# Performance work log

Measured on AMD Instinct MI355X. Metric: run time of the kernel, lower is better.

The kernel has to match this reference:

```python
import jax, jax.numpy as jnp
import numpy as np

CTX, SP, HIST, NC = 168, 24, 336, 128
LAGS = [24, 48, 72, 96, 120, 144, 168, 0]  # lags_seq + [0]
NSEG = CTX // SP  # 7


def gru_cell(x, h, Wih, Whh, bih, bhh):
    # torch.nn.GRUCell math; x: (N, D), h: (N, H)
    gi = x @ Wih.T + bih
    gh = h @ Whh.T + bhh
    ir, iz, inn = jnp.split(gi, 3, axis=-1)
    hr, hz, hn = jnp.split(gh, 3, axis=-1)
    r = jax.nn.sigmoid(ir + hr)
    z = jax.nn.sigmoid(iz + hz)
    n = jnp.tanh(inn + r * hn)
    return (1.0 - z) * n + z * h


def lstm(x, h, c, Wih, Whh, b):
    # single-layer batch_first LSTM; x: (B, T, D); torch gate order i,f,g,o
    xw = jnp.einsum('btd,gd->btg', x, Wih) + b  # precompute input projection
    def step(carry, xt):
        h, c = carry
        gates = xt + h @ Whh.T
        i, f, g, o = jnp.split(gates, 4, axis=-1)
        c = jax.nn.sigmoid(f) * c + jax.nn.sigmoid(i) * jnp.tanh(g)
        h = jax.nn.sigmoid(o) * jnp.tanh(c)
        return (h, c), h
    (h, c), ys = jax.lax.scan(step, (h, c), jnp.swapaxes(xw, 0, 1))
    return jnp.swapaxes(ys, 0, 1), h, c


def setup_inputs() -> dict:
    key = jax.random.key(0)
    ks = jax.random.split(key, 20)
    B = 8192
    p = lambda k, shape: jax.random.normal(k, shape, jnp.float32) * 0.05
    return dict(
        feat_static_cat=jax.random.randint(ks[0], (B, 1), 0, 50),
        feat_static_real=jax.random.normal(ks[1], (B, 1), jnp.float32),
        past_time_feat=jax.random.normal(ks[2], (B, HIST, 4), jnp.float32),
        past_target=jax.random.uniform(ks[3], (B, HIST), jnp.float32),
        past_observed_values=jnp.ones((B, HIST), jnp.float32),
        future_time_feat=jax.random.normal(ks[4], (B, SP, 4), jnp.float32),
        emb_table=p(ks[5], (50, 16)),
        gru_Wih=p(ks[6], (3 * NC, 30)),
        gru_Whh=p(ks[7], (3 * NC, NC)),
        gru_bih=p(ks[8], (3 * NC,)),
        gru_bhh=p(ks[9], (3 * NC,)),
        enc_Wih=p(ks[10], (NSEG, 4 * NC, NC)),
        enc_Whh=p(ks[11], (NSEG, 4 * NC, NC)),
        enc_b=p(ks[12], (NSEG, 4 * NC)),
        dec_Wih=p(ks[13], (4 * NC, 180)),
        dec_Whh=p(ks[14], (4 * NC, NC)),
        dec_b=p(ks[15], (4 * NC,)),
        out_W=p(ks[16], (1, NC)),
        out_b=p(ks[17], (1,)),
    )


def reference(feat_static_cat, feat_static_real, past_time_feat, past_target,
              past_observed_values, future_time_feat,
              emb_table, gru_Wih, gru_Whh, gru_bih, gru_bhh,
              enc_Wih, enc_Whh, enc_b, dec_Wih, dec_Whh, dec_b,
              out_W, out_b):
    B = past_target.shape[0]
    time_feat = past_time_feat[:, HIST - CTX:, :]  # (B, CTX, 4)

    # lagged subsequences: lagged[:, j, k] = seq[:, HIST - lag_k - CTX + j]
    lags = jnp.stack(
        [past_target[:, HIST - lag - CTX: HIST - lag] for lag in LAGS], axis=-1
    )  # (B, CTX, 8)

    # MeanScaler over past_target[:, CTX:] (keepdim)
    data = past_target[:, CTX:]
    w = past_observed_values[:, CTX:]
    total_w = w.sum(axis=1)                     # (B,)
    wsum = (jnp.abs(data) * w).sum(axis=1)      # (B,)
    default_scale = wsum.sum() / jnp.maximum(total_w.sum(), 1.0)
    scale = wsum / jnp.maximum(total_w, 1.0)
    scale = jnp.maximum(1e-10, jnp.where(wsum > 0, scale, default_scale))
    scale = scale[:, None]                      # (B, 1)

    embedded = emb_table[feat_static_cat[:, 0]]  # (B, 16)
    static_feat = jnp.concatenate([embedded, feat_static_real, jnp.log(scale)], axis=1)  # (B, 18)
    rep_static = jnp.broadcast_to(static_feat[:, None, :], (B, CTX, static_feat.shape[-1]))

    lags_scaled = lags / scale[:, :, None]
    inputs = jnp.concatenate([lags_scaled, time_feat, rep_static], axis=-1)  # (B, CTX, 30)
    inputs = inputs.reshape(B, NSEG, SP, inputs.shape[-1])  # (B, 7, 24, 30)

    encoder_out = jnp.zeros((B, SP, NC), inputs.dtype)
    h = jnp.zeros((B, NC), inputs.dtype)
    c = jnp.zeros((B, NC), inputs.dtype)
    for i in range(NSEG):  # fixed small loop; each segment has distinct LSTM weights
        x = inputs[:, i].reshape(-1, inputs.shape[-1])  # (B*SP, 30)
        hv = gru_cell(x, encoder_out.reshape(-1, NC), gru_Wih, gru_Whh, gru_bih, gru_bhh)
        hv = hv.reshape(B, SP, NC)
        encoder_out, h, c = lstm(hv, h, c, enc_Wih[i], enc_Whh[i], enc_b[i])

    query = jnp.concatenate(
        [inputs[:, 0], encoder_out, future_time_feat, rep_static[:, -SP:, :]], axis=-1
    )  # (B, 24, 180)
    dec_out, _, _ = lstm(query, h, c, dec_Wih, dec_Whh, dec_b)
    outputs = dec_out @ out_W.T + out_b  # (B, 24, 1)
    return outputs * scale[:, :, None]
```

## Files before the change

### kernel.cpp

```cpp
#include <hip/hip_runtime.h>
#include <math.h>

typedef short bf16x8 __attribute__((ext_vector_type(8)));
typedef float f32x4 __attribute__((ext_vector_type(4)));
typedef unsigned short u16;
typedef unsigned int u32;

#define WSUMS 0
#define TOTWS 1
#define WSUM_OFF 2
#define TOTW_OFF 8194
#define SCL_F 16386
#define WB_BYTE 98432

#define GWI_U 0
#define GWH_U 12288
#define EO_U  61440
#define DO_U  978944
#define XG_U  1142784
#define XD_U  23162880

#define L2E 1.4426950408889634f
#define T2E 2.8853900817779268f

__constant__ int cLAG[8] = {144,120,96,72,48,24,0,168};

__device__ __forceinline__ float sig2(float x){
  return __builtin_amdgcn_rcpf(1.0f+__builtin_amdgcn_exp2f(-x));
}
__device__ __forceinline__ float th2(float x){
  return __builtin_fmaf(-2.0f, __builtin_amdgcn_rcpf(__builtin_amdgcn_exp2f(x)+1.0f), 1.0f);
}
__device__ __forceinline__ float thc(float x){
  return th2(x*T2E);
}
__device__ __forceinline__ u16 f2b(float x){ u32 u=__float_as_uint(x); return (u16)((u + 0x7fffu + ((u>>16)&1u))>>16); }
__device__ __forceinline__ float b2f(u16 v){ return __uint_as_float(((u32)v)<<16); }
__device__ __forceinline__ u32 f2b_pk(float lo, float hi){
  u32 r; asm("v_cvt_pk_bf16_f32 %0, %1, %2" : "=v"(r) : "v"(lo), "v"(hi)); return r;
}
__device__ __forceinline__ void pin(bf16x8 &x){
  f32x4 t = __builtin_bit_cast(f32x4, x);
  asm volatile("" : "+v"(t));
  x = __builtin_bit_cast(bf16x8, t);
}

#define MFMA(a,b,c) __builtin_amdgcn_mfma_f32_16x16x32_bf16(a,b,c,0,0,0)

__global__ void scale_kernel(const float* __restrict__ tgt,
                             const float* __restrict__ obs,
                             float* __restrict__ ws)
{
  __shared__ float s1[256], s2[256];
  int b = blockIdx.x*256 + threadIdx.x;
  float wsum=0.f, totw=0.f;
  const float* tr = tgt + b*336 + 168;
  const float* wr = obs + b*336 + 168;
  for(int t=0;t<168;t++){ float w=wr[t]; wsum += fabsf(tr[t])*w; totw += w; }
  ws[WSUM_OFF + b] = wsum;
  ws[TOTW_OFF + b] = totw;
  s1[threadIdx.x]=wsum; s2[threadIdx.x]=totw;
  __syncthreads();
  for(int s=128;s>0;s>>=1){
    if(threadIdx.x<s){ s1[threadIdx.x]+=s1[threadIdx.x+s]; s2[threadIdx.x]+=s2[threadIdx.x+s]; }
    __syncthreads();
  }
  if(threadIdx.x==0){ atomicAdd(&ws[WSUMS], s1[0]); atomicAdd(&ws[TOTWS], s2[0]); }
}

__global__ void prep_w(const float* __restrict__ gWih, const float* __restrict__ gWhh,
                       const float* __restrict__ eWih, const float* __restrict__ eWhh,
                       const float* __restrict__ dWih, const float* __restrict__ dWhh,
                       float* __restrict__ ws)
{
  u16* WU = (u16*)((char*)ws + WB_BYTE);
  int tid = blockIdx.x*blockDim.x + threadIdx.x;
  int nt = gridDim.x*blockDim.x;
  for(int i=tid;i<12288;i+=nt){ int n=i>>5,k=i&31;
    float s=((n>>7)==2)?T2E:L2E;
    WU[GWI_U+i]=(k<30)?f2b(gWih[n*30+k]*s):(u16)0; }
  for(int i=tid;i<49152;i+=nt){ int n=i>>7,k=i&127;
    float s=((n>>7)==2)?T2E:L2E;
    WU[GWH_U+i]=f2b(gWhh[n*128+k]*s); }
  for(int i=tid;i<917504;i+=nt){
    int s=i>>17,r2=i&131071,n=r2>>8,k=r2&255;
    float sc=((n>>7)==2)?T2E:L2E;
    float v=(k<128)?eWih[(s*512+n)*128+k]:eWhh[(s*512+n)*128+(k-128)];
    WU[EO_U+i]=f2b(v*sc);
  }
  for(int i=tid;i<163840;i+=nt){
    int n=i/320, k=i-n*320; float v;
    float sc=((n>>7)==2)?T2E:L2E;
    if(k<128)       v=dWih[n*180+30+k];
    else if(k<136)  v=dWih[n*180+(k-128)];
    else if(k<140)  v=dWih[n*180+8+(k-136)];
    else if(k<144)  v=dWih[n*180+158+(k-140)];
    else if(k<162)  v=dWih[n*180+12+(k-144)];
    else if(k<180)  v=dWih[n*180+162+(k-162)];
    else if(k<192)  v=0.f;
    else            v=dWhh[n*128+(k-192)];
    WU[DO_U+i]=f2b(v*sc);
  }
}

__global__ void prep_x(const float* __restrict__ tgt, const float* __restrict__ ptf,
                       const float* __restrict__ ftf, float* __restrict__ ws)
{
  __shared__ float inv_l[64];
  u16* WU = (u16*)((char*)ws + WB_BYTE);
  const int tid = threadIdx.x;
  const int b0 = blockIdx.x*64;
  if(tid<64){
    int b=b0+tid;
    float wsumv=ws[WSUM_OFF+b], totw=ws[TOTW_OFF+b];
    float def=ws[WSUMS]/fmaxf(ws[TOTWS],1.f);
    float sc=fmaxf(1e-10f,(wsumv>0.f)?wsumv/fmaxf(totw,1.f):def);
    ws[SCL_F+b]=sc; inv_l[tid]=1.f/sc;
  }
  __syncthreads();
  for(int idx=tid; idx<64*168; idx+=256){
    int bl=idx/168, gt=idx-bl*168; int b=b0+bl;
    float iv=inv_l[bl];
    __align__(16) u16 row[16];
    #pragma unroll
    for(int j=0;j<8;j++) row[j]=f2b(tgt[b*336+cLAG[j]+gt]*iv);
    const float* pp=ptf+((size_t)(b*336+168+gt))*4;
    #pragma unroll
    for(int j=0;j<4;j++) row[8+j]=f2b(pp[j]);
    row[12]=row[13]=row[14]=row[15]=0;
    int seg=gt/24, t=gt-seg*24;
    u16* dst=WU+XG_U+(((size_t)seg*8192+b)*24+t)*16;
    *(uint4*)dst=*(const uint4*)row; *(uint4*)(dst+8)=*(const uint4*)(row+8);
  }
  for(int idx=tid; idx<64*24; idx+=256){
    int bl=idx/24, t=idx-bl*24; int b=b0+bl;
    float iv=inv_l[bl];
    __align__(16) u16 row[16];
    #pragma unroll
    for(int j=0;j<8;j++) row[j]=f2b(tgt[b*336+cLAG[j]+t]*iv);
    #pragma unroll
    for(int j=0;j<4;j++) row[8+j]=f2b(ptf[((size_t)(b*336+168+t))*4+j]);
    #pragma unroll
    for(int j=0;j<4;j++) row[12+j]=f2b(ftf[b*96+t*4+j]);
    u16* dst=WU+XD_U+((size_t)b*24+t)*16;
    *(uint4*)dst=*(const uint4*)row; *(uint4*)(dst+8)=*(const uint4*)(row+8);
  }
}

__global__ __launch_bounds__(512,2)
__attribute__((amdgpu_waves_per_eu(2,2)))
void deepar_main(const int* __restrict__ cat, const float* __restrict__ sreal,
                 const float* __restrict__ emb,
                 const float* __restrict__ gbih, const float* __restrict__ gbhh,
                 const float* __restrict__ encb, const float* __restrict__ decb,
                 const float* __restrict__ outW, const float* __restrict__ outb,
                 float* __restrict__ ws, float* __restrict__ out)
{
  asm volatile("" ::: "v252","v253","v254","v255");

  const u16* __restrict__ WU=(const u16*)((const char*)ws+WB_BYTE);

  __shared__ __align__(16) u16 encbuf[384*136];
  __shared__ __align__(16) u16 Xast[4][64*40];
  __shared__ __align__(16) u16 Xdast[2][16*72];
  __shared__ __align__(16) u16 hstash[2][16*136];
  __shared__ u16 statb[16][18];
  __shared__ float scl_s[16];
  __shared__ float outw_s[128];
  __shared__ float red[16][8];
  __shared__ float outb_s;

  const int tid=threadIdx.x;
  const int b0=blockIdx.x*16;
  const int wv=tid>>6, lane=tid&63, quad=lane>>4, l15=lane&15;
  const int ccol=wv*16+quad*4;

  auto stageX = [&](int gc){
    if(tid<128 && gc<42){
      int sg=gc/6, cc=gc-sg*6;
      int a=tid>>1;
      u16* Xb=&Xast[gc&3][0];
      const u16* src=WU+XG_U+(((size_t)sg*8192+b0+(a>>2))*24+4*cc+(a&3))*16;
      if(tid&1) *(uint2*)(Xb+a*40+8)=*(const uint2*)(src+8);
      else      *(uint4*)(Xb+a*40)  =*(const uint4*)src;
    }
  };

  if(tid<16) scl_s[tid]=ws[SCL_F+b0+tid];
  if(tid<128) outw_s[tid]=outW[tid];
  if(tid==128) outb_s=outb[0];
  if(tid>=256){ int q=tid-256; int r=q>>4,k=q&15; statb[r][k]=f2b(emb[cat[b0+r]*16+k]); }
  { const uint4 z4={0,0,0,0};
    for(int i=tid;i<6528;i+=512) *(uint4*)(encbuf+i*8)=z4;
    for(int i=tid;i<544;i+=512)  *(uint4*)(&hstash[0][0]+i*8)=z4;
  }
  __syncthreads();
  if(tid<16){ statb[tid][16]=f2b(sreal[b0+tid]); statb[tid][17]=f2b(logf(scl_s[tid])); }
  __syncthreads();
  for(int i=tid;i<1280;i+=512){ int a=i/20, k=i-a*20+12;
    u16 v=(k<30)?statb[a>>2][k-12]:(u16)0;
    Xast[0][a*40+k]=v; Xast[1][a*40+k]=v; Xast[2][a*40+k]=v; Xast[3][a*40+k]=v; }
  for(int i=tid;i<896;i+=512){ int rr=i/56, k=i-rr*56+16;
    u16 v; if(k<34) v=statb[rr][k-16]; else if(k<52) v=statb[rr][k-34]; else v=0;
    Xdast[0][rr*72+k]=v; Xdast[1][rr*72+k]=v; }
  stageX(0); stageX(1);
  __syncthreads();

  f32x4 b4r, b4z, b4i2, b4h2;
  {
    float4 bi0=*(const float4*)(gbih+(wv    )*16+quad*4);
    float4 bh0=*(const float4*)(gbhh+(wv    )*16+quad*4);
    float4 bi1=*(const float4*)(gbih+(wv+ 8)*16+quad*4);
    float4 bh1=*(const float4*)(gbhh+(wv+ 8)*16+quad*4);
    float4 bi2=*(const float4*)(gbih+(wv+16)*16+quad*4);
    float4 bh2=*(const float4*)(gbhh+(wv+16)*16+quad*4);
    b4r =(f32x4){(bi0.x+bh0.x)*L2E,(bi0.y+bh0.y)*L2E,(bi0.z+bh0.z)*L2E,(bi0.w+bh0.w)*L2E};
    b4z =(f32x4){(bi1.x+bh1.x)*L2E,(bi1.y+bh1.y)*L2E,(bi1.z+bh1.z)*L2E,(bi1.w+bh1.w)*L2E};
    b4i2=(f32x4){bi2.x*T2E,bi2.y*T2E,bi2.z*T2E,bi2.w*T2E};
    b4h2=(f32x4){bh2.x*T2E,bh2.y*T2E,bh2.z*T2E,bh2.w*T2E};
  }

  float cst[4]={0.f,0.f,0.f,0.f};
  int p=0;

  for(int seg=0;seg<7;seg++){
    bf16x8 gwi[3]; bf16x8 gwh[3][4];
    #pragma unroll
    for(int j=0;j<3;j++){
      int nb=(wv+j*8)*16+l15;
      gwi[j]=*(const bf16x8*)(WU+GWI_U+nb*32+quad*8); pin(gwi[j]);
      #pragma unroll
      for(int kt=0;kt<4;kt++){ gwh[j][kt]=*(const bf16x8*)(WU+GWH_U+nb*128+kt*32+quad*8); pin(gwh[j][kt]); }
    }

    for(int c=0;c<6;c++){
      stageX(seg*6+c+2);
      const u16* Xb = &Xast[(seg*6+c)&3][0];

      f32x4 g01[2][4], a2[4], h2[4];
      #pragma unroll
      for(int mt=0;mt<4;mt++){
        bf16x8 af=*(const bf16x8*)(Xb+(mt*16+l15)*40+quad*8);
        g01[0][mt]=MFMA(gwi[0],af,b4r);
        g01[1][mt]=MFMA(gwi[1],af,b4z);
        a2[mt]   =MFMA(gwi[2],af,b4i2);
      }
      const u16* ebase=encbuf+(size_t)(c*64)*136;
      #pragma unroll
      for(int kt=0;kt<4;kt++)
        #pragma unroll
        for(int mt=0;mt<4;mt++){
          bf16x8 af=*(const bf16x8*)(ebase+(mt*16+l15)*136+kt*32+quad*8);
          g01[0][mt]=MFMA(gwh[0][kt],af,g01[0][mt]);
          g01[1][mt]=MFMA(gwh[1][kt],af,g01[1][mt]);
          h2[mt]   =MFMA(gwh[2][kt],af,(kt==0)?b4h2:h2[mt]);
        }
      uint2 hv2[4];
      #pragma unroll
      for(int mt=0;mt<4;mt++){
        uint2 hp2=*(const uint2*)(ebase+(size_t)(mt*16+l15)*136+ccol);
        float hv[4];
        #pragma unroll
        for(int reg=0;reg<4;reg++){
          float rg=sig2(g01[0][mt][reg]);
          float zg=sig2(g01[1][mt][reg]);
          u32 w=(reg&2)?hp2.y:hp2.x;
          float hp=b2f((u16)((reg&1)?(w>>16):w));
          float nn=th2(__builtin_fmaf(rg,h2[mt][reg],a2[mt][reg]));
          hv[reg]=__builtin_fmaf(zg,hp-nn,nn);
        }
        hv2[mt].x=f2b_pk(hv[0],hv[1]);
        hv2[mt].y=f2b_pk(hv[2],hv[3]);
      }
      __syncthreads();
      #pragma unroll
      for(int mt=0;mt<4;mt++)
        *(uint2*)(encbuf+(size_t)(c*64+mt*16+l15)*136+ccol)=hv2[mt];
    }

    bf16x8 we[4][8]; f32x4 b4e[4];
    #pragma unroll
    for(int j=0;j<4;j++){
      float s=(j==2)?T2E:L2E;
      float4 bb=*(const float4*)(encb+seg*512+(wv+j*8)*16+quad*4);
      b4e[j]=(f32x4){bb.x*s,bb.y*s,bb.z*s,bb.w*s};
      int nb=(wv+j*8)*16+l15;
      #pragma unroll
      for(int kt=0;kt<8;kt++){
        we[j][kt]=*(const bf16x8*)(WU+EO_U+(size_t)seg*131072+nb*256+kt*32+quad*8);
        pin(we[j][kt]);
      }
    }
    uint2 hprev2={0,0}; int tbprev=0;
    for(int t=0;t<24;t++){
      int tb=(t>>2)*64+(t&3);
      __syncthreads();
      const u16* Hb=&hstash[p][0];
      const u16* Ar=encbuf+(size_t)(tb+l15*4)*136;
      f32x4 acc[4];
      #pragma unroll
      for(int kt=0;kt<8;kt++){
        bf16x8 af=(kt<4)? *(const bf16x8*)(Ar+kt*32+quad*8)
                        : *(const bf16x8*)(Hb+l15*136+(kt-4)*32+quad*8);
        #pragma unroll
        for(int j=0;j<4;j++) acc[j]=MFMA(we[j][kt],af,(kt==0)?b4e[j]:acc[j]);
      }
      if(t>0)
        *(uint2*)(encbuf+(size_t)(tbprev+l15*4)*136+ccol)=hprev2;
      { float hf[4];
        #pragma unroll
        for(int reg=0;reg<4;reg++){
          float ig=sig2(acc[0][reg]),fg=sig2(acc[1][reg]);
          float gg=th2(acc[2][reg]), og=sig2(acc[3][reg]);
          float c_=__builtin_fmaf(fg,cst[reg],ig*gg); cst[reg]=c_;
          hf[reg]=og*thc(c_);
        }
        hprev2.x=f2b_pk(hf[0],hf[1]);
        hprev2.y=f2b_pk(hf[2],hf[3]);
      }
      int pn=p^1;
      *(uint2*)(&hstash[pn][0]+(size_t)l15*136+ccol)=hprev2;
      tbprev=tb; p=pn;
    }
    *(uint2*)(encbuf+(size_t)(tbprev+l15*4)*136+ccol)=hprev2;
  }

  bf16x8 wd[4][10]; f32x4 b4d[4];
  #pragma unroll
  for(int j=0;j<4;j++){
    float s=(j==2)?T2E:L2E;
    float4 bb=*(const float4*)(decb+(wv+j*8)*16+quad*4);
    b4d[j]=(f32x4){bb.x*s,bb.y*s,bb.z*s,bb.w*s};
    int nb=(wv+j*8)*16+l15;
    #pragma unroll
    for(int kt=0;kt<10;kt++){
      wd[j][kt]=*(const bf16x8*)(WU+DO_U+nb*320+kt*32+quad*8);
      pin(wd[j][kt]);
    }
  }
  if(tid>=256 && tid<288){ int q=tid-256; int rr=q>>1;
    const u16* src=WU+XD_U+((size_t)(b0+rr)*24+0)*16;
    u16* Xw=&Xdast[0][0];
    if(q&1) *(uint4*)(Xw+rr*72+8)=*(const uint4*)(src+8);
    else    *(uint4*)(Xw+rr*72)  =*(const uint4*)src; }
  __syncthreads();
  for(int t=0;t<24;t++){
    int tb=(t>>2)*64+(t&3);
    const u16* Ar=encbuf+(size_t)(tb+l15*4)*136;
    const u16* Xd=&Xdast[t&1][0];
    const u16* Hb=&hstash[p][0];
    f32x4 acc[4];
    #pragma unroll
    for(int kt=0;kt<10;kt++){
      bf16x8 af=(kt<4)? *(const bf16x8*)(Ar+kt*32+quad*8)
              :(kt<6)? *(const bf16x8*)(Xd+l15*72+(kt-4)*32+quad*8)
                     : *(const bf16x8*)(Hb+l15*136+(kt-6)*32+quad*8);
      #pragma unroll
      for(int j=0;j<4;j++) acc[j]=MFMA(wd[j][kt],af,(kt==0)?b4d[j]:acc[j]);
    }
    if(t<23 && tid>=256 && tid<288){ int q=tid-256; int rr=q>>1;
      const u16* src=WU+XD_U+((size_t)(b0+rr)*24+t+1)*16;
      u16* Xw=&Xdast[(t+1)&1][0];
      if(q&1) *(uint4*)(Xw+rr*72+8)=*(const uint4*)(src+8);
      else    *(uint4*)(Xw+rr*72)  =*(const uint4*)src; }
    uint2 hnew2;
    { float hf[4];
      #pragma unroll
      for(int reg=0;reg<4;reg++){
        float ig=sig2(acc[0][reg]),fg=sig2(acc[1][reg]);
        float gg=th2(acc[2][reg]), og=sig2(acc[3][reg]);
        float c_=__builtin_fmaf(fg,cst[reg],ig*gg); cst[reg]=c_;
        hf[reg]=og*thc(c_);
      }
      hnew2.x=f2b_pk(hf[0],hf[1]);
      hnew2.y=f2b_pk(hf[2],hf[3]);
    }
    int pn=p^1;
    *(uint2*)(&hstash[pn][0]+(size_t)l15*136+ccol)=hnew2;
    __syncthreads();
    if(tid<128){ int row=tid>>3,g=tid&7; float s=0.f;
      #pragma unroll
      for(int i=0;i<16;i++) s+=b2f(hstash[pn][row*136+g*16+i])*outw_s[g*16+i];
      red[row][g]=s; }
    __syncthreads();
    if(tid<16){ float s=outb_s;
      #pragma unroll
      for(int g=0;g<8;g++) s+=red[tid][g];
      out[(b0+tid)*24+t]=s*scl_s[tid]; }
    p=pn;
  }
}

extern "C" void kernel_launch(void* const* d_in, const int* in_sizes, int n_in,
                              void* d_out, int out_size, void* d_ws, size_t ws_size,
                              hipStream_t stream)
{
  (void)in_sizes; (void)n_in; (void)out_size; (void)ws_size;
  const int*   cat  = (const int*)d_in[0];
  const float* sreal= (const float*)d_in[1];
  const float* ptf  = (const float*)d_in[2];
  const float* tgt  = (const float*)d_in[3];
  const float* obs  = (const float*)d_in[4];
  const float* ftf  = (const float*)d_in[5];
  const float* emb  = (const float*)d_in[6];
  const float* gWih = (const float*)d_in[7];
  const float* gWhh = (const float*)d_in[8];
  const float* gbih = (const float*)d_in[9];
  const float* gbhh = (const float*)d_in[10];
  const float* eWih = (const float*)d_in[11];
  const float* eWhh = (const float*)d_in[12];
  const float* encb = (const float*)d_in[13];
  const float* dWih = (const float*)d_in[14];
  const float* dWhh = (const float*)d_in[15];
  const float* decb = (const float*)d_in[16];
  const float* outW = (const float*)d_in[17];
  const float* outb = (const float*)d_in[18];
  float* ws  = (float*)d_ws;
  float* out = (float*)d_out;

  hipMemsetAsync(d_ws, 0, 2*sizeof(float), stream);
  scale_kernel<<<dim3(8192/256), dim3(256), 0, stream>>>(tgt, obs, ws);
  prep_w<<<dim3(512), dim3(256), 0, stream>>>(gWih,gWhh,eWih,eWhh,dWih,dWhh,ws);
  prep_x<<<dim3(128), dim3(256), 0, stream>>>(tgt, ptf, ftf, ws);
  deepar_main<<<dim3(512), dim3(512), 0, stream>>>(cat,sreal,emb,gbih,gbhh,encb,decb,
                                                   outW,outb,ws,out);
}
```

Before: 897.3 us.

## Split LSTM gate accumulators, pad LDS rows, fuse output projection into gate epilogue

Widens the LDS row stride for encbuf and hstash from 136 to 140 elements, meant to cut bank conflicts on the fragment loads. In the encoder and decoder LSTM steps, the single serial MFMA accumulation chain is split into two independent chains (input part and hidden part) that are summed before the gates, giving more instruction-level parallelism. The decoder output projection now uses per-thread fp32 partial dot products written to a double-buffered reduction array, which removes one __syncthreads and the separate reduction pass per step. It costs a few extra adds, more LDS, and a slightly different fp32 (not bf16-rounded) output sum.

Result: slower. 1.499 ms (+67.1%).

```diff
diff --git a/kernel.cpp b/kernel.cpp
--- a/kernel.cpp
+++ b/kernel.cpp
@@ -22,6 +22,8 @@
 
 #define L2E 1.4426950408889634f
 #define T2E 2.8853900817779268f
+
+#define EROW 140
 
 __constant__ int cLAG[8] = {144,120,96,72,48,24,0,168};
 
@@ -160,20 +162,20 @@
 
   const u16* __restrict__ WU=(const u16*)((const char*)ws+WB_BYTE);
 
-  __shared__ __align__(16) u16 encbuf[384*136];
+  __shared__ __align__(16) u16 encbuf[384*EROW];
   __shared__ __align__(16) u16 Xast[4][64*40];
   __shared__ __align__(16) u16 Xdast[2][16*72];
-  __shared__ __align__(16) u16 hstash[2][16*136];
+  __shared__ __align__(16) u16 hstash[2][16*EROW];
   __shared__ u16 statb[16][18];
   __shared__ float scl_s[16];
-  __shared__ float outw_s[128];
-  __shared__ float red[16][8];
+  __shared__ float red2[2][16][32];
   __shared__ float outb_s;
 
   const int tid=threadIdx.x;
   const int b0=blockIdx.x*16;
   const int wv=tid>>6, lane=tid&63, quad=lane>>4, l15=lane&15;
   const int ccol=wv*16+quad*4;
+  const f32x4 zz={0.f,0.f,0.f,0.f};
 
   auto stageX = [&](int gc){
     if(tid<128 && gc<42){
@@ -187,13 +189,13 @@
   };
 
   if(tid<16) scl_s[tid]=ws[SCL_F+b0+tid];
-  if(tid<128) outw_s[tid]=outW[tid];
   if(tid==128) outb_s=outb[0];
   if(tid>=256){ int q=tid-256; int r=q>>4,k=q&15; statb[r][k]=f2b(emb[cat[b0+r]*16+k]); }
   { const uint4 z4={0,0,0,0};
-    for(int i=tid;i<6528;i+=512) *(uint4*)(encbuf+i*8)=z4;
-    for(int i=tid;i<544;i+=512)  *(uint4*)(&hstash[0][0]+i*8)=z4;
-  }
+    for(int i=tid;i<6720;i+=512) *(uint4*)(encbuf+i*8)=z4;
+    for(int i=tid;i<560;i+=512)  *(uint4*)(&hstash[0][0]+i*8)=z4;
+  }
+  const float4 ow=*(const float4*)(outW+ccol);
   __syncthreads();
   if(tid<16){ statb[tid][16]=f2b(sreal[b0+tid]); statb[tid][17]=f2b(logf(scl_s[tid])); }
   __syncthreads();
@@ -245,12 +247,12 @@
         g01[1][mt]=MFMA(gwi[1],af,b4z);
         a2[mt]   =MFMA(gwi[2],af,b4i2);
       }
-      const u16* ebase=encbuf+(size_t)(c*64)*136;
+      const u16* ebase=encbuf+(size_t)(c*64)*EROW;
       #pragma unroll
       for(int kt=0;kt<4;kt++)
         #pragma unroll
         for(int mt=0;mt<4;mt++){
-          bf16x8 af=*(const bf16x8*)(ebase+(mt*16+l15)*136+kt*32+quad*8);
+          bf16x8 af=*(const bf16x8*)(ebase+(mt*16+l15)*EROW+kt*32+quad*8);
           g01[0][mt]=MFMA(gwh[0][kt],af,g01[0][mt]);
           g01[1][mt]=MFMA(gwh[1][kt],af,g01[1][mt]);
           h2[mt]   =MFMA(gwh[2][kt],af,(kt==0)?b4h2:h2[mt]);
@@ -258,7 +260,7 @@
       uint2 hv2[4];
       #pragma unroll
       for(int mt=0;mt<4;mt++){
-        uint2 hp2=*(const uint2*)(ebase+(size_t)(mt*16+l15)*136+ccol);
+        uint2 hp2=*(const uint2*)(ebase+(size_t)(mt*16+l15)*EROW+ccol);
         float hv[4];
         #pragma unroll
         for(int reg=0;reg<4;reg++){
@@ -275,7 +277,7 @@
       __syncthreads();
       #pragma unroll
       for(int mt=0;mt<4;mt++)
-        *(uint2*)(encbuf+(size_t)(c*64+mt*16+l15)*136+ccol)=hv2[mt];
+        *(uint2*)(encbuf+(size_t)(c*64+mt*16+l15)*EROW+ccol)=hv2[mt];
     }
 
     bf16x8 we[4][8]; f32x4 b4e[4];
@@ -296,22 +298,27 @@
       int tb=(t>>2)*64+(t&3);
       __syncthreads();
       const u16* Hb=&hstash[p][0];
-      const u16* Ar=encbuf+(size_t)(tb+l15*4)*136;
-      f32x4 acc[4];
-      #pragma unroll
-      for(int kt=0;kt<8;kt++){
-        bf16x8 af=(kt<4)? *(const bf16x8*)(Ar+kt*32+quad*8)
-                        : *(const bf16x8*)(Hb+l15*136+(kt-4)*32+quad*8);
+      const u16* Ar=encbuf+(size_t)(tb+l15*4)*EROW;
+      f32x4 aA[4], aH[4];
+      #pragma unroll
+      for(int kt=0;kt<4;kt++){
+        bf16x8 afA=*(const bf16x8*)(Ar+kt*32+quad*8);
+        bf16x8 afH=*(const bf16x8*)(Hb+l15*EROW+kt*32+quad*8);
         #pragma unroll
-        for(int j=0;j<4;j++) acc[j]=MFMA(we[j][kt],af,(kt==0)?b4e[j]:acc[j]);
+        for(int j=0;j<4;j++){
+          aA[j]=MFMA(we[j][kt],afA,(kt==0)?b4e[j]:aA[j]);
+          aH[j]=MFMA(we[j][kt+4],afH,(kt==0)?zz:aH[j]);
+        }
       }
       if(t>0)
-        *(uint2*)(encbuf+(size_t)(tbprev+l15*4)*136+ccol)=hprev2;
+        *(uint2*)(encbuf+(size_t)(tbprev+l15*4)*EROW+ccol)=hprev2;
       { float hf[4];
         #pragma unroll
         for(int reg=0;reg<4;reg++){
-          float ig=sig2(acc[0][reg]),fg=sig2(acc[1][reg]);
-          float gg=th2(acc[2][reg]), og=sig2(acc[3][reg]);
+          float a0=aA[0][reg]+aH[0][reg], a1=aA[1][reg]+aH[1][reg];
+          float a2v=aA[2][reg]+aH[2][reg], a3=aA[3][reg]+aH[3][reg];
+          float ig=sig2(a0),fg=sig2(a1);
+          float gg=th2(a2v), og=sig2(a3);
           float c_=__builtin_fmaf(fg,cst[reg],ig*gg); cst[reg]=c_;
           hf[reg]=og*thc(c_);
         }
@@ -319,10 +326,10 @@
         hprev2.y=f2b_pk(hf[2],hf[3]);
       }
       int pn=p^1;
-      *(uint2*)(&hstash[pn][0]+(size_t)l15*136+ccol)=hprev2;
+      *(uint2*)(&hstash[pn][0]+(size_t)l15*EROW+ccol)=hprev2;
       tbprev=tb; p=pn;
     }
-    *(uint2*)(encbuf+(size_t)(tbprev+l15*4)*136+ccol)=hprev2;
+    *(uint2*)(encbuf+(size_t)(tbprev+l15*4)*EROW+ccol)=hprev2;
   }
 
   bf16x8 wd[4][10]; f32x4 b4d[4];
@@ -346,17 +353,21 @@
   __syncthreads();
   for(int t=0;t<24;t++){
     int tb=(t>>2)*64+(t&3);
-    const u16* Ar=encbuf+(size_t)(tb+l15*4)*136;
+    const u16* Ar=encbuf+(size_t)(tb+l15*4)*EROW;
     const u16* Xd=&Xdast[t&1][0];
     const u16* Hb=&hstash[p][0];
-    f32x4 acc[4];
-    #pragma unroll
-    for(int kt=0;kt<10;kt++){
-      bf16x8 af=(kt<4)? *(const bf16x8*)(Ar+kt*32+quad*8)
-              :(kt<6)? *(const bf16x8*)(Xd+l15*72+(kt-4)*32+quad*8)
-                     : *(const bf16x8*)(Hb+l15*136+(kt-6)*32+quad*8);
-      #pragma unroll
-      for(int j=0;j<4;j++) acc[j]=MFMA(wd[j][kt],af,(kt==0)?b4d[j]:acc[j]);
+    f32x4 aA[4], aH[4];
+    #pragma unroll
+    for(int kt=0;kt<5;kt++){
+      bf16x8 afA=(kt<4)? *(const bf16x8*)(Ar+kt*32+quad*8)
+                       : *(const bf16x8*)(Xd+l15*72+quad*8);
+      bf16x8 afH=(kt<1)? *(const bf16x8*)(Xd+l15*72+32+quad*8)
+                       : *(const bf16x8*)(Hb+l15*EROW+(kt-1)*32+quad*8);
+      #pragma unroll
+      for(int j=0;j<4;j++){
+        aA[j]=MFMA(wd[j][kt],afA,(kt==0)?b4d[j]:aA[j]);
+        aH[j]=MFMA(wd[j][kt+5],afH,(kt==0)?zz:aH[j]);
+      }
     }
     if(t<23 && tid>=256 && tid<288){ int q=tid-256; int rr=q>>1;
       const u16* src=WU+XD_U+((size_t)(b0+rr)*24+t+1)*16;
@@ -367,25 +378,25 @@
     { float hf[4];
       #pragma unroll
       for(int reg=0;reg<4;reg++){
-        float ig=sig2(acc[0][reg]),fg=sig2(acc[1][reg]);
-        float gg=th2(acc[2][reg]), og=sig2(acc[3][reg]);
+        float a0=aA[0][reg]+aH[0][reg], a1=aA[1][reg]+aH[1][reg];
+        float a2v=aA[2][reg]+aH[2][reg], a3=aA[3][reg]+aH[3][reg];
+        float ig=sig2(a0),fg=sig2(a1);
+        float gg=th2(a2v), og=sig2(a3);
         float c_=__builtin_fmaf(fg,cst[reg],ig*gg); cst[reg]=c_;
         hf[reg]=og*thc(c_);
       }
+      float part=hf[0]*ow.x; part=__builtin_fmaf(hf[1],ow.y,part);
+      part=__builtin_fmaf(hf[2],ow.z,part); part=__builtin_fmaf(hf[3],ow.w,part);
+      red2[t&1][l15][wv*4+quad]=part;
       hnew2.x=f2b_pk(hf[0],hf[1]);
       hnew2.y=f2b_pk(hf[2],hf[3]);
     }
     int pn=p^1;
-    *(uint2*)(&hstash[pn][0]+(size_t)l15*136+ccol)=hnew2;
-    __syncthreads();
-    if(tid<128){ int row=tid>>3,g=tid&7; float s=0.f;
-      #pragma unroll
-      for(int i=0;i<16;i++) s+=b2f(hstash[pn][row*136+g*16+i])*outw_s[g*16+i];
-      red[row][g]=s; }
+    *(uint2*)(&hstash[pn][0]+(size_t)l15*EROW+ccol)=hnew2;
     __syncthreads();
     if(tid<16){ float s=outb_s;
       #pragma unroll
-      for(int g=0;g<8;g++) s+=red[tid][g];
+      for(int g=0;g<32;g++) s+=red2[t&1][tid][g];
       out[(b0+tid)*24+t]=s*scl_s[tid]; }
     p=pn;
   }
```
